# Optimization experiments

Measured on AMD Instinct MI355X. Metric: run time of the kernel, lower is better.

## Reference

```python
import jax, jax.numpy as jnp
import numpy as np

B, S, D, H, DH = 2, 2048, 1024, 16, 64
SCALE = float(np.sqrt(DH))
IGNORE = -100000.0


def setup_inputs() -> dict:
    key = jax.random.key(0)
    ks = jax.random.split(key, 9)
    s = 0.02
    return {
        "x": jax.random.normal(ks[0], (B, S, D), dtype=jnp.float32),
        "W_Q": jax.random.normal(ks[1], (H, DH, D), dtype=jnp.float32) * s,
        "W_K": jax.random.normal(ks[2], (H, DH, D), dtype=jnp.float32) * s,
        "W_V": jax.random.normal(ks[3], (H, DH, D), dtype=jnp.float32) * s,
        "W_O": jax.random.normal(ks[4], (H, D, DH), dtype=jnp.float32) * s,
        "b_Q": jax.random.normal(ks[5], (H, DH), dtype=jnp.float32) * s,
        "b_K": jax.random.normal(ks[6], (H, DH), dtype=jnp.float32) * s,
        "b_V": jax.random.normal(ks[7], (H, DH), dtype=jnp.float32) * s,
        "b_O": jax.random.normal(ks[8], (D,), dtype=jnp.float32) * s,
        "mask": jnp.tril(jnp.ones((S, S), dtype=bool)),  # causal, global attn_type
    }


def reference(x, W_Q, W_K, W_V, W_O, b_Q, b_K, b_V, b_O, mask):
    # q,k,v: [batch, pos, head, d_head]
    q = jnp.einsum('ihm,bpm->bpih', W_Q, x) + b_Q
    k = jnp.einsum('ihm,bpm->bpih', W_K, x) + b_K
    v = jnp.einsum('ihm,bpm->bpih', W_V, x) + b_V
    # scores: [batch, head, q_pos, k_pos]
    attn_scores = jnp.einsum('bpih,bqih->bipq', q, k) / SCALE
    attn_scores = jnp.where(mask, attn_scores, IGNORE)
    attn = jax.nn.softmax(attn_scores, axis=-1)
    # z: [batch, q_pos, head, d_head]
    z = jnp.einsum('bpih,biqp->bqih', v, attn)
    out = jnp.einsum('idh,bqih->bqd', W_O, z) + b_O
    return out
```

## Files before the change

kernel.cpp:

```cpp
#include <hip/hip_runtime.h>
#include <stdint.h>

typedef __attribute__((ext_vector_type(8))) short bf16x8;
typedef __attribute__((ext_vector_type(4))) float f32x4;
typedef __attribute__((ext_vector_type(16))) float f32x16;
typedef __attribute__((ext_vector_type(4))) unsigned short us4;

#define LOG2E 1.44269504088896340736f

__device__ __forceinline__ unsigned short f2bf(float f) {
    union { float f; unsigned u; } v; v.f = f;
    unsigned r = v.u + 0x7FFFu + ((v.u >> 16) & 1u);
    return (unsigned short)(r >> 16);
}
__device__ __forceinline__ float bf2f(unsigned short u) {
    return __uint_as_float(((unsigned)u) << 16);
}

__device__ __forceinline__ unsigned cvtpk(float lo, float hi) {
    unsigned r;
    asm("v_cvt_pk_bf16_f32 %0, %1, %2" : "=v"(r) : "v"(lo), "v"(hi));
    return r;
}
__device__ __forceinline__ void plswap(unsigned &a, unsigned &b) {
    asm volatile("v_permlane32_swap_b32 %0, %1" : "+v"(a), "+v"(b));
}

__device__ __forceinline__ void gld16(const void* g, void* l) {
    __builtin_amdgcn_global_load_lds((const __attribute__((address_space(1))) void*)g,
                                     (__attribute__((address_space(3))) void*)l, 16, 0, 0);
}

__global__ void k_cvt(const float* __restrict__ in, unsigned short* __restrict__ out, int n4) {
    int i = blockIdx.x * blockDim.x + threadIdx.x;
    if (i >= n4) return;
    float4 v = ((const float4*)in)[i];
    us4 o; o.x = f2bf(v.x); o.y = f2bf(v.y); o.z = f2bf(v.z); o.w = f2bf(v.w);
    *(us4*)(out + (size_t)i * 4) = o;
}

__global__ void k_cvt3(const float* __restrict__ a, const float* __restrict__ b,
                       const float* __restrict__ cc,
                       unsigned short* __restrict__ oa, unsigned short* __restrict__ ob,
                       unsigned short* __restrict__ oc) {
    const float* in = blockIdx.y == 0 ? a : (blockIdx.y == 1 ? b : cc);
    unsigned short* out = blockIdx.y == 0 ? oa : (blockIdx.y == 1 ? ob : oc);
    int i = blockIdx.x * blockDim.x + threadIdx.x;
    float4 v = ((const float4*)in)[i];
    us4 o; o.x = f2bf(v.x); o.y = f2bf(v.y); o.z = f2bf(v.z); o.w = f2bf(v.w);
    *(us4*)(out + (size_t)i * 4) = o;
}

__global__ void k_cvt_wo(const float* __restrict__ WO, unsigned short* __restrict__ out) {
    int t = blockIdx.x * blockDim.x + threadIdx.x;
    int d = t >> 10, nn = t & 1023, i = nn >> 6, h = nn & 63;
    out[t] = f2bf(WO[(((size_t)i << 10) + d) * 64 + h]);
}

__global__ __launch_bounds__(256) void k_gemm_qkv(
    const unsigned short* __restrict__ Xb,
    const unsigned short* __restrict__ Wq, const unsigned short* __restrict__ Wk,
    const unsigned short* __restrict__ Wv,
    const float* __restrict__ bQ, const float* __restrict__ bK, const float* __restrict__ bV,
    unsigned short* __restrict__ Qb, unsigned short* __restrict__ Kb, unsigned short* __restrict__ VTb)
{
    __shared__ unsigned short As[128][128];
    __shared__ unsigned short Bs[128][128];
    const int which = blockIdx.z;
    const unsigned short* Wp = which == 0 ? Wq : (which == 1 ? Wk : Wv);
    const int bm = blockIdx.x, bn = blockIdx.y;
    const int t = threadIdx.x, lane = t & 63, wave = t >> 6;
    const int wm = wave >> 1, wn = wave & 1;
    const int l15 = lane & 15, l4 = lane >> 4;
    const int rsw = l15 & 7;
    const int c0 = wave * 64 + lane;
    const int arow = bm << 7, brow = bn << 7;
    f32x4 acc[4][4] = {};

    for (int k0 = 0; k0 < 1024; k0 += 128) {
        #pragma unroll
        for (int it = 0; it < 8; ++it) {
            int c = it * 256 + c0;
            int row = c >> 4, sl = (c & 15) ^ (row & 7);
            gld16(Xb + ((size_t)(arow + row)) * 1024 + k0 + sl * 8, (char*)As + (c << 4));
            gld16(Wp + ((size_t)(brow + row)) * 1024 + k0 + sl * 8, (char*)Bs + (c << 4));
        }
        __syncthreads();
        const char* Ab = (const char*)As;
        const char* Bb = (const char*)Bs;
        #pragma unroll
        for (int kk = 0; kk < 4; ++kk) {
            bf16x8 af[4], bfg[4];
            #pragma unroll
            for (int m = 0; m < 4; ++m)
                af[m] = *(const bf16x8*)(Ab + (wm * 64 + m * 16 + l15) * 256 + (((kk * 4 + l4) ^ rsw) << 4));
            #pragma unroll
            for (int n = 0; n < 4; ++n)
                bfg[n] = *(const bf16x8*)(Bb + (wn * 64 + n * 16 + l15) * 256 + (((kk * 4 + l4) ^ rsw) << 4));
            __builtin_amdgcn_s_setprio(1);
            #pragma unroll
            for (int m = 0; m < 4; ++m)
                #pragma unroll
                for (int n = 0; n < 4; ++n)
                    acc[m][n] = __builtin_amdgcn_mfma_f32_16x16x32_bf16(af[m], bfg[n], acc[m][n], 0, 0, 0);
            __builtin_amdgcn_s_setprio(0);
        }
        __syncthreads();
    }
    #pragma unroll
    for (int m = 0; m < 4; ++m) {
        #pragma unroll
        for (int n = 0; n < 4; ++n) {
            int col = (bn << 7) + wn * 64 + n * 16 + l15;
            int i = col >> 6, h = col & 63;
            float bias = which == 0 ? bQ[col] : (which == 1 ? bK[col] : bV[col]);
            #pragma unroll
            for (int r = 0; r < 4; ++r) {
                int p = (bm << 7) + wm * 64 + m * 16 + (l4 << 2) + r;
                int b = p >> 11, s = p & 2047;
                float v = acc[m][n][r] + bias;
                if (which == 0)
                    Qb[(((((size_t)b << 4) + i) << 11) + s) * 64 + h] = f2bf(v * (0.125f * LOG2E));
                else if (which == 1)
                    Kb[(((((size_t)b << 4) + i) << 11) + s) * 64 + h] = f2bf(v);
                else
                    VTb[(((((size_t)b << 4) + i) << 6) + h) * 2048 + s] = f2bf(v);
            }
        }
    }
}

__global__ __launch_bounds__(128) void k_attn(
    const unsigned short* __restrict__ Qb, const unsigned short* __restrict__ Kb,
    const unsigned short* __restrict__ VTb,
    unsigned short* __restrict__ Zp, float* __restrict__ Lse)
{
    __shared__ __align__(16) char Lbuf[16384];
    const int id = (int)blockIdx.x;
    const int bi = id & 31;
    const int r = id >> 5;
    const int c = 31 - (r >> 1);
    const int part = r & 1;
    const int n = c + 1, n0 = (n + 1) >> 1;
    const int t0 = part ? n0 : 0, t1 = part ? n : n0;
    const int lane = threadIdx.x & 63, w = threadIdx.x >> 6;
    const int l31 = lane & 31, hi = lane >> 5;
    const unsigned short* Qh = Qb + (size_t)bi * 2048 * 64;
    const char* Khb = (const char*)(Kb + (size_t)bi * 2048 * 64);
    const char* Vhb = (const char*)(VTb + (size_t)bi * 64 * 2048);
    const int q0 = c * 64 + w * 32;
    const int q = q0 + l31;

    bf16x8 qf[4];
    #pragma unroll
    for (int kk = 0; kk < 4; ++kk)
        qf[kk] = *(const bf16x8*)&Qh[(size_t)q * 64 + kk * 16 + hi * 8];

    const int r8 = lane >> 3;
    const int swz = ((lane & 7) * 16) ^ (r8 << 4);
    const int koff = r8 * 128 + swz;
    const int voff = r8 * 4096 + swz;

    const int rsw = (l31 & 7) << 4;
    int kaddr[8];
    #pragma unroll
    for (int i = 0; i < 8; ++i)
        kaddr[i] = (l31 + 32 * (i >> 2)) * 128 + ((32 * (i & 3) + 16 * hi) ^ rsw);
    int vcol[4];
    #pragma unroll
    for (int f = 0; f < 4; ++f)
        vcol[f] = ((f * 32 + 16 * hi) ^ rsw);

    f32x16 za0 = {}, za1 = {};
    float m_run = -1e30f, l_run = 0.f;

    if (t0 < t1) {
        if (w == 0) {
            const char* src = Khb + (size_t)t0 * 8192 + koff;
            #pragma unroll
            for (int it = 0; it < 8; ++it) gld16(src + it * 1024, &Lbuf[0] + it * 1024);
        } else {
            const char* src = Vhb + (size_t)t0 * 128 + voff;
            #pragma unroll
            for (int it = 0; it < 8; ++it) gld16(src + it * 32768, &Lbuf[8192] + it * 1024);
        }
    }

    for (int t = t0; t < t1; ++t) {
        __syncthreads();
        const char* KL = &Lbuf[0];
        const char* VL = &Lbuf[8192];
        bf16x8 ka[8];
        #pragma unroll
        for (int i = 0; i < 8; ++i) ka[i] = *(const bf16x8*)(KL + kaddr[i]);
        bf16x8 vf0[4], vf1[4];
        #pragma unroll
        for (int f = 0; f < 4; ++f) {
            vf0[f] = *(const bf16x8*)(VL + l31 * 128 + vcol[f]);
            vf1[f] = *(const bf16x8*)(VL + (l31 + 32) * 128 + vcol[f]);
        }
        __syncthreads();
        if (t + 1 < t1) {
            if (w == 0) {
                const char* src = Khb + (size_t)(t + 1) * 8192 + koff;
                #pragma unroll
                for (int it = 0; it < 8; ++it) gld16(src + it * 1024, &Lbuf[0] + it * 1024);
            } else {
                const char* src = Vhb + (size_t)(t + 1) * 128 + voff;
                #pragma unroll
                for (int it = 0; it < 8; ++it) gld16(src + it * 32768, &Lbuf[8192] + it * 1024);
            }
        }

        const bool full = !(t == c && w == 0);
        f32x16 s0 = {}, s1;
        __builtin_amdgcn_s_setprio(1);
        #pragma unroll
        for (int kk = 0; kk < 4; ++kk)
            s0 = __builtin_amdgcn_mfma_f32_32x32x16_bf16(ka[kk], qf[kk], s0, 0, 0, 0);
        if (full) {
            f32x16 z = {};
            #pragma unroll
            for (int kk = 0; kk < 4; ++kk)
                z = __builtin_amdgcn_mfma_f32_32x32x16_bf16(ka[4 + kk], qf[kk], z, 0, 0, 0);
            s1 = z;
        }
        __builtin_amdgcn_s_setprio(0);

        if (!full) {
            #pragma unroll
            for (int j = 0; j < 16; ++j) s1[j] = -100000.0f;
        }
        if (t == c) {
            #pragma unroll
            for (int j = 0; j < 16; ++j) {
                int kv0 = (j & 3) + 8 * (j >> 2) + 4 * hi;
                if (c * 64 + kv0 > q) s0[j] = -100000.0f;
                if (c * 64 + kv0 + 32 > q) s1[j] = -100000.0f;
            }
        }
        float tmax = -1e30f;
        #pragma unroll
        for (int j = 0; j < 16; ++j) tmax = fmaxf(tmax, fmaxf(s0[j], s1[j]));
        tmax = fmaxf(tmax, __shfl_xor(tmax, 32, 64));
        if (!__all(tmax <= m_run + 8.0f)) {
            float newm = fmaxf(m_run, tmax);
            float alpha = exp2f(m_run - newm);
            m_run = newm;
            l_run *= alpha;
            za0 *= alpha; za1 *= alpha;
        }
        float rsum = 0.f;
        #pragma unroll
        for (int j = 0; j < 16; ++j) { s0[j] = exp2f(s0[j] - m_run); rsum += s0[j]; }
        if (full) {
            #pragma unroll
            for (int j = 0; j < 16; ++j) { s1[j] = exp2f(s1[j] - m_run); rsum += s1[j]; }
        }
        rsum += __shfl_xor(rsum, 32, 64);
        l_run += rsum;

        union { unsigned u[4]; bf16x8 v; } pk0, pk1, pk2, pk3;
        {
            unsigned a0 = cvtpk(s0[0], s0[1]),  a1 = cvtpk(s0[2], s0[3]);
            unsigned a2 = cvtpk(s0[4], s0[5]),  a3 = cvtpk(s0[6], s0[7]);
            plswap(a0, a2); plswap(a1, a3);
            pk0.u[0] = a0; pk0.u[1] = a1; pk0.u[2] = a2; pk0.u[3] = a3;
            unsigned b0 = cvtpk(s0[8], s0[9]),  b1 = cvtpk(s0[10], s0[11]);
            unsigned b2 = cvtpk(s0[12], s0[13]), b3 = cvtpk(s0[14], s0[15]);
            plswap(b0, b2); plswap(b1, b3);
            pk1.u[0] = b0; pk1.u[1] = b1; pk1.u[2] = b2; pk1.u[3] = b3;
        }
        if (full) {
            unsigned a0 = cvtpk(s1[0], s1[1]),  a1 = cvtpk(s1[2], s1[3]);
            unsigned a2 = cvtpk(s1[4], s1[5]),  a3 = cvtpk(s1[6], s1[7]);
            plswap(a0, a2); plswap(a1, a3);
            pk2.u[0] = a0; pk2.u[1] = a1; pk2.u[2] = a2; pk2.u[3] = a3;
            unsigned b0 = cvtpk(s1[8], s1[9]),  b1 = cvtpk(s1[10], s1[11]);
            unsigned b2 = cvtpk(s1[12], s1[13]), b3 = cvtpk(s1[14], s1[15]);
            plswap(b0, b2); plswap(b1, b3);
            pk3.u[0] = b0; pk3.u[1] = b1; pk3.u[2] = b2; pk3.u[3] = b3;
        }
        __builtin_amdgcn_s_setprio(1);
        za0 = __builtin_amdgcn_mfma_f32_32x32x16_bf16(vf0[0], pk0.v, za0, 0, 0, 0);
        za1 = __builtin_amdgcn_mfma_f32_32x32x16_bf16(vf1[0], pk0.v, za1, 0, 0, 0);
        za0 = __builtin_amdgcn_mfma_f32_32x32x16_bf16(vf0[1], pk1.v, za0, 0, 0, 0);
        za1 = __builtin_amdgcn_mfma_f32_32x32x16_bf16(vf1[1], pk1.v, za1, 0, 0, 0);
        if (full) {
            za0 = __builtin_amdgcn_mfma_f32_32x32x16_bf16(vf0[2], pk2.v, za0, 0, 0, 0);
            za1 = __builtin_amdgcn_mfma_f32_32x32x16_bf16(vf1[2], pk2.v, za1, 0, 0, 0);
            za0 = __builtin_amdgcn_mfma_f32_32x32x16_bf16(vf0[3], pk3.v, za0, 0, 0, 0);
            za1 = __builtin_amdgcn_mfma_f32_32x32x16_bf16(vf1[3], pk3.v, za1, 0, 0, 0);
        }
        __builtin_amdgcn_s_setprio(0);
    }

    const float rl = (l_run > 0.f) ? 1.0f / l_run : 0.f;
    const float lse = (l_run > 0.f) ? m_run + log2f(l_run) : -1e30f;
    const int pb = (part << 5) + bi;
    unsigned short* zp = Zp + ((size_t)pb * 2048 + q) * 64;
    #pragma unroll
    for (int nn = 0; nn < 2; ++nn) {
        #pragma unroll
        for (int gg = 0; gg < 4; ++gg) {
            int dh0 = nn * 32 + 8 * gg + 4 * hi;
            us4 o;
            float v0 = (nn ? za1[4 * gg + 0] : za0[4 * gg + 0]) * rl;
            float v1 = (nn ? za1[4 * gg + 1] : za0[4 * gg + 1]) * rl;
            float v2 = (nn ? za1[4 * gg + 2] : za0[4 * gg + 2]) * rl;
            float v3 = (nn ? za1[4 * gg + 3] : za0[4 * gg + 3]) * rl;
            o.x = f2bf(v0); o.y = f2bf(v1); o.z = f2bf(v2); o.w = f2bf(v3);
            *(us4*)(zp + dh0) = o;
        }
    }
    if (hi == 0) Lse[(size_t)pb * 2048 + q] = lse;
}

__global__ __launch_bounds__(256) void k_combine(
    const unsigned short* __restrict__ Zp, const float* __restrict__ Lse,
    unsigned short* __restrict__ Zb)
{
    const int tid = blockIdx.x * 256 + threadIdx.x;
    const int dc = tid & 7, q = (tid >> 3) & 2047, bi = tid >> 14;
    const float l0 = Lse[(size_t)bi * 2048 + q];
    const float l1 = Lse[(size_t)(32 + bi) * 2048 + q];
    const float M = fmaxf(l0, l1);
    float e0 = exp2f(l0 - M), e1 = exp2f(l1 - M);
    const float rs = 1.0f / (e0 + e1);
    e0 *= rs; e1 *= rs;
    const size_t base = ((size_t)bi * 2048 + q) * 64 + dc * 8;
    bf16x8 z0 = *(const bf16x8*)(Zp + base);
    bf16x8 z1 = *(const bf16x8*)(Zp + (size_t)32 * 2048 * 64 + base);
    const int b = bi >> 4, ih = bi & 15;
    unsigned short* op = Zb + (((size_t)b * 2048 + q) << 10) + ih * 64 + dc * 8;
    bf16x8 o;
    #pragma unroll
    for (int j = 0; j < 8; ++j) {
        float v = e0 * bf2f((unsigned short)z0[j]) + e1 * bf2f((unsigned short)z1[j]);
        o[j] = (short)f2bf(v);
    }
    *(bf16x8*)op = o;
}

__global__ __launch_bounds__(256) void k_gemm_out(
    const unsigned short* __restrict__ Zb, const unsigned short* __restrict__ Wo,
    const float* __restrict__ bO, float* __restrict__ out)
{
    __shared__ unsigned short As[128][128];
    __shared__ unsigned short Bs[128][128];
    const int bm = blockIdx.x, bn = blockIdx.y;
    const int t = threadIdx.x, lane = t & 63, wave = t >> 6;
    const int wm = wave >> 1, wn = wave & 1;
    const int l15 = lane & 15, l4 = lane >> 4;
    const int rsw = l15 & 7;
    const int c0 = wave * 64 + lane;
    const int arow = bm << 7, brow = bn << 7;
    f32x4 acc[4][4] = {};

    for (int k0 = 0; k0 < 1024; k0 += 128) {
        #pragma unroll
        for (int it = 0; it < 8; ++it) {
            int c = it * 256 + c0;
            int row = c >> 4, sl = (c & 15) ^ (row & 7);
            gld16(Zb + ((size_t)(arow + row)) * 1024 + k0 + sl * 8, (char*)As + (c << 4));
            gld16(Wo + ((size_t)(brow + row)) * 1024 + k0 + sl * 8, (char*)Bs + (c << 4));
        }
        __syncthreads();
        const char* Ab = (const char*)As;
        const char* Bb = (const char*)Bs;
        #pragma unroll
        for (int kk = 0; kk < 4; ++kk) {
            bf16x8 af[4], bfg[4];
            #pragma unroll
            for (int m = 0; m < 4; ++m)
                af[m] = *(const bf16x8*)(Ab + (wm * 64 + m * 16 + l15) * 256 + (((kk * 4 + l4) ^ rsw) << 4));
            #pragma unroll
            for (int n = 0; n < 4; ++n)
                bfg[n] = *(const bf16x8*)(Bb + (wn * 64 + n * 16 + l15) * 256 + (((kk * 4 + l4) ^ rsw) << 4));
            __builtin_amdgcn_s_setprio(1);
            #pragma unroll
            for (int m = 0; m < 4; ++m)
                #pragma unroll
                for (int n = 0; n < 4; ++n)
                    acc[m][n] = __builtin_amdgcn_mfma_f32_16x16x32_bf16(af[m], bfg[n], acc[m][n], 0, 0, 0);
            __builtin_amdgcn_s_setprio(0);
        }
        __syncthreads();
    }
    #pragma unroll
    for (int m = 0; m < 4; ++m) {
        #pragma unroll
        for (int n = 0; n < 4; ++n) {
            int col = (bn << 7) + wn * 64 + n * 16 + l15;
            float bias = bO[col];
            #pragma unroll
            for (int r = 0; r < 4; ++r) {
                int p = (bm << 7) + wm * 64 + m * 16 + (l4 << 2) + r;
                out[(size_t)p * 1024 + col] = acc[m][n][r] + bias;
            }
        }
    }
}

extern "C" void kernel_launch(void* const* d_in, const int* in_sizes, int n_in,
                              void* d_out, int out_size, void* d_ws, size_t ws_size,
                              hipStream_t stream)
{
    const float* x  = (const float*)d_in[0];
    const float* WQ = (const float*)d_in[1];
    const float* WK = (const float*)d_in[2];
    const float* WV = (const float*)d_in[3];
    const float* WO = (const float*)d_in[4];
    const float* bQ = (const float*)d_in[5];
    const float* bK = (const float*)d_in[6];
    const float* bV = (const float*)d_in[7];
    const float* bO = (const float*)d_in[8];
    float* out = (float*)d_out;

    char* w = (char*)d_ws;
    unsigned short* xb  = (unsigned short*)w; w += (size_t)4096 * 1024 * 2;
    unsigned short* wqb = (unsigned short*)w; w += (size_t)1024 * 1024 * 2;
    unsigned short* wkb = (unsigned short*)w; w += (size_t)1024 * 1024 * 2;
    unsigned short* wvb = (unsigned short*)w; w += (size_t)1024 * 1024 * 2;
    unsigned short* wob = (unsigned short*)w; w += (size_t)1024 * 1024 * 2;
    unsigned short* Qb  = (unsigned short*)w; w += (size_t)4096 * 1024 * 2;
    unsigned short* Kb  = (unsigned short*)w; w += (size_t)4096 * 1024 * 2;
    unsigned short* VTb = (unsigned short*)w; w += (size_t)4096 * 1024 * 2;
    unsigned short* Zb  = (unsigned short*)w; w += (size_t)4096 * 1024 * 2;
    unsigned short* Zp  = (unsigned short*)w; w += (size_t)2 * 32 * 2048 * 64 * 2;
    float*          Lse = (float*)w;          w += (size_t)2 * 32 * 2048 * 4;

    k_cvt<<<4096, 256, 0, stream>>>(x, xb, 1048576);
    k_cvt3<<<dim3(1024, 3), 256, 0, stream>>>(WQ, WK, WV, wqb, wkb, wvb);
    k_cvt_wo<<<4096, 256, 0, stream>>>(WO, wob);

    k_gemm_qkv<<<dim3(32, 8, 3), 256, 0, stream>>>(xb, wqb, wkb, wvb, bQ, bK, bV, Qb, Kb, VTb);
    k_attn<<<2048, 128, 0, stream>>>(Qb, Kb, VTb, Zp, Lse);
    k_combine<<<2048, 256, 0, stream>>>(Zp, Lse, Zb);
    k_gemm_out<<<dim3(32, 8), 256, 0, stream>>>(Zb, wob, bO, out);
}
```

Measured before the change: 129.9 us.

## Split attention KV range into fixed 8-tile chunks with variable split count

Replaces the fixed two-way KV split per query tile with chunks of at most 8 KV tiles, so longer causal rows get up to four partitions while short rows get one. This balances per-block work and removes the empty-partition guards. The combine kernel now merges a variable number of partials (1-4) by log-sum-exp. It costs more partial output traffic and a larger workspace, plus 2560 attention blocks instead of 2048.

```diff
diff --git a/kernel.cpp b/kernel.cpp
--- a/kernel.cpp
+++ b/kernel.cpp
@@ -138,11 +138,15 @@
     __shared__ __align__(16) char Lbuf[16384];
     const int id = (int)blockIdx.x;
     const int bi = id & 31;
-    const int r = id >> 5;
-    const int c = 31 - (r >> 1);
-    const int part = r & 1;
-    const int n = c + 1, n0 = (n + 1) >> 1;
-    const int t0 = part ? n0 : 0, t1 = part ? n : n0;
+    const int g = 79 - (id >> 5);
+    int c, p;
+    if (g < 8)       { c = g;                  p = 0; }
+    else if (g < 24) { int u = g - 8;  c = 8  + (u >> 1); p = u & 1; }
+    else if (g < 48) { int u = g - 24; c = 16 + u / 3;    p = u % 3; }
+    else             { int u = g - 48; c = 24 + (u >> 2); p = u & 3; }
+    const int t0 = p << 3;
+    const int te = t0 + 8, cp1 = c + 1;
+    const int t1 = te < cp1 ? te : cp1;
     const int lane = threadIdx.x & 63, w = threadIdx.x >> 6;
     const int l31 = lane & 31, hi = lane >> 5;
     const unsigned short* Qh = Qb + (size_t)bi * 2048 * 64;
@@ -174,16 +178,14 @@
     f32x16 za0 = {}, za1 = {};
     float m_run = -1e30f, l_run = 0.f;
 
-    if (t0 < t1) {
-        if (w == 0) {
-            const char* src = Khb + (size_t)t0 * 8192 + koff;
-            #pragma unroll
-            for (int it = 0; it < 8; ++it) gld16(src + it * 1024, &Lbuf[0] + it * 1024);
-        } else {
-            const char* src = Vhb + (size_t)t0 * 128 + voff;
-            #pragma unroll
-            for (int it = 0; it < 8; ++it) gld16(src + it * 32768, &Lbuf[8192] + it * 1024);
-        }
+    if (w == 0) {
+        const char* src = Khb + (size_t)t0 * 8192 + koff;
+        #pragma unroll
+        for (int it = 0; it < 8; ++it) gld16(src + it * 1024, &Lbuf[0] + it * 1024);
+    } else {
+        const char* src = Vhb + (size_t)t0 * 128 + voff;
+        #pragma unroll
+        for (int it = 0; it < 8; ++it) gld16(src + it * 32768, &Lbuf[8192] + it * 1024);
     }
 
     for (int t = t0; t < t1; ++t) {
@@ -295,9 +297,9 @@
         __builtin_amdgcn_s_setprio(0);
     }
 
-    const float rl = (l_run > 0.f) ? 1.0f / l_run : 0.f;
-    const float lse = (l_run > 0.f) ? m_run + log2f(l_run) : -1e30f;
-    const int pb = (part << 5) + bi;
+    const float rl = 1.0f / l_run;
+    const float lse = m_run + log2f(l_run);
+    const int pb = (p << 5) + bi;
     unsigned short* zp = Zp + ((size_t)pb * 2048 + q) * 64;
     #pragma unroll
     for (int nn = 0; nn < 2; ++nn) {
@@ -322,23 +324,28 @@
 {
     const int tid = blockIdx.x * 256 + threadIdx.x;
     const int dc = tid & 7, q = (tid >> 3) & 2047, bi = tid >> 14;
-    const float l0 = Lse[(size_t)bi * 2048 + q];
-    const float l1 = Lse[(size_t)(32 + bi) * 2048 + q];
-    const float M = fmaxf(l0, l1);
-    float e0 = exp2f(l0 - M), e1 = exp2f(l1 - M);
-    const float rs = 1.0f / (e0 + e1);
-    e0 *= rs; e1 *= rs;
-    const size_t base = ((size_t)bi * 2048 + q) * 64 + dc * 8;
-    bf16x8 z0 = *(const bf16x8*)(Zp + base);
-    bf16x8 z1 = *(const bf16x8*)(Zp + (size_t)32 * 2048 * 64 + base);
+    const int c = q >> 6, np = (c + 8) >> 3;
+    float l[4], M = -1e30f;
+    for (int pp = 0; pp < np; ++pp) {
+        l[pp] = Lse[(size_t)((pp << 5) + bi) * 2048 + q];
+        M = fmaxf(M, l[pp]);
+    }
+    float e[4], s = 0.f;
+    for (int pp = 0; pp < np; ++pp) { e[pp] = exp2f(l[pp] - M); s += e[pp]; }
+    const float rs = 1.0f / s;
+    float acc[8] = {};
+    for (int pp = 0; pp < np; ++pp) {
+        const float wgt = e[pp] * rs;
+        const size_t base = ((size_t)((pp << 5) + bi) * 2048 + q) * 64 + dc * 8;
+        bf16x8 z = *(const bf16x8*)(Zp + base);
+        #pragma unroll
+        for (int j = 0; j < 8; ++j) acc[j] += wgt * bf2f((unsigned short)z[j]);
+    }
     const int b = bi >> 4, ih = bi & 15;
     unsigned short* op = Zb + (((size_t)b * 2048 + q) << 10) + ih * 64 + dc * 8;
     bf16x8 o;
     #pragma unroll
-    for (int j = 0; j < 8; ++j) {
-        float v = e0 * bf2f((unsigned short)z0[j]) + e1 * bf2f((unsigned short)z1[j]);
-        o[j] = (short)f2bf(v);
-    }
+    for (int j = 0; j < 8; ++j) o[j] = (short)f2bf(acc[j]);
     *(bf16x8*)op = o;
 }
 
@@ -427,15 +434,15 @@
     unsigned short* Kb  = (unsigned short*)w; w += (size_t)4096 * 1024 * 2;
     unsigned short* VTb = (unsigned short*)w; w += (size_t)4096 * 1024 * 2;
     unsigned short* Zb  = (unsigned short*)w; w += (size_t)4096 * 1024 * 2;
-    unsigned short* Zp  = (unsigned short*)w; w += (size_t)2 * 32 * 2048 * 64 * 2;
-    float*          Lse = (float*)w;          w += (size_t)2 * 32 * 2048 * 4;
+    unsigned short* Zp  = (unsigned short*)w; w += (size_t)4 * 32 * 2048 * 64 * 2;
+    float*          Lse = (float*)w;          w += (size_t)4 * 32 * 2048 * 4;
 
     k_cvt<<<4096, 256, 0, stream>>>(x, xb, 1048576);
     k_cvt3<<<dim3(1024, 3), 256, 0, stream>>>(WQ, WK, WV, wqb, wkb, wvb);
     k_cvt_wo<<<4096, 256, 0, stream>>>(WO, wob);
 
     k_gemm_qkv<<<dim3(32, 8, 3), 256, 0, stream>>>(xb, wqb, wkb, wvb, bQ, bK, bV, Qb, Kb, VTb);
-    k_attn<<<2048, 128, 0, stream>>>(Qb, Kb, VTb, Zp, Lse);
+    k_attn<<<2560, 128, 0, stream>>>(Qb, Kb, VTb, Zp, Lse);
     k_combine<<<2048, 256, 0, stream>>>(Zp, Lse, Zb);
     k_gemm_out<<<dim3(32, 8), 256, 0, stream>>>(Zb, wob, bO, out);
 }
```

Result: slower. 136.2 us (+4.9%).
